# Kernel optimization log

Hardware: AMD Instinct MI355X
Metric: run time of the kernel (lower is better)

The kernel has to match this reference:

```python
import jax, jax.numpy as jnp
import numpy as np

B, L, N, H, HU = 512, 16, 10000, 128, 128

def _rn(k, shape, s=0.05):
    return jax.random.normal(k, shape, jnp.float32) * s

def setup_inputs():
    ks = jax.random.split(jax.random.key(0), 26)
    return dict(
        x=jax.random.normal(ks[0], (B, 2), jnp.float32),
        t0_res=jax.random.normal(ks[1], (B, 1), jnp.float32),
        node_inputs=jax.random.normal(ks[2], (B, 2 * L, N), jnp.float32),
        tau_inputs=jax.random.normal(ks[3], (B, L, 1), jnp.float32),
        end=jax.random.normal(ks[4], (B, 2), jnp.float32),
        coords=jax.random.normal(ks[5], (B, 2 * L, 2), jnp.float32),
        Wx1=_rn(ks[6], (1, 2)), Wx2=_rn(ks[7], (H, 1)), bx2=_rn(ks[8], (H,)),
        Wres=_rn(ks[9], (H, 1)), bres=_rn(ks[10], (H,)),
        Wnode=_rn(ks[11], (H, N)),
        Wtau=_rn(ks[12], (H, 1)), btau=_rn(ks[13], (H,)),
        Wend1=_rn(ks[14], (1, 2)), Wend2=_rn(ks[15], (H, 1)), bend2=_rn(ks[16], (H,)),
        Wcoord=_rn(ks[17], (H, 2)),
        lstm_Wih=_rn(ks[18], (7, 4 * H, H)), lstm_Whh=_rn(ks[19], (7, 4 * H, H)),
        lstm_bih=_rn(ks[20], (7, 4 * H)), lstm_bhh=_rn(ks[21], (7, 4 * H)),
        head_W1=_rn(ks[22], (7, HU, H)), head_b1=_rn(ks[23], (7, HU)),
        head_W2=_rn(ks[24], (7, 1, HU)), head_b2=_rn(ks[25], (7, 1)),
    )

def _lstm_last(s, Wih, Whh, bih, bhh):
    # s: [T, B, H] (time-first, like torch LSTM default). PyTorch gate order: i, f, g, o.
    h0 = jnp.zeros((s.shape[1], Whh.shape[1]), s.dtype)
    def step(carry, xt):
        h, c = carry
        g = xt @ Wih.T + h @ Whh.T + (bih + bhh)
        i, f, gg, o = jnp.split(g, 4, axis=-1)
        c = jax.nn.sigmoid(f) * c + jax.nn.sigmoid(i) * jnp.tanh(gg)
        h = jax.nn.sigmoid(o) * jnp.tanh(c)
        return (h, c), None
    (h, _), _ = jax.lax.scan(step, (h0, h0), s)
    return h  # last output == last hidden state

def _forward(x, t0_res, node_inputs, tau_inputs, end, coords,
             Wx1, Wx2, bx2, Wres, bres, Wnode, Wtau, btau,
             Wend1, Wend2, bend2, Wcoord,
             lstm_Wih, lstm_Whh, lstm_bih, lstm_bhh,
             head_W1, head_b1, head_W2, head_b2):
    xh = jnp.tanh((x @ Wx1.T) @ Wx2.T + bx2)        # [B,H]
    t0h = jnp.tanh(t0_res @ Wres.T + bres)          # [B,H]
    nodeh = node_inputs @ Wnode.T                   # [B,2L,H] (dominant memory-bound GEMM)
    tauh = jnp.tanh(tau_inputs @ Wtau.T + btau)     # [B,L,H]
    endh = (end @ Wend1.T) @ Wend2.T + bend2        # [B,H]
    coordh = coords @ Wcoord.T                      # [B,2L,H]
    ne, no = nodeh[:, 0::2], nodeh[:, 1::2]         # even/odd walk nodes [B,L,H]
    ce, co = coordh[:, 0::2], coordh[:, 1::2]
    def interleave(parts):  # k x [B,L,H] -> time-first [k*L, B, H], per-step order preserved
        s = jnp.stack(parts, axis=2)
        return jnp.swapaxes(s.reshape(s.shape[0], -1, s.shape[-1]), 0, 1)
    pre = jnp.stack([xh, t0h], axis=0)  # [2,B,H]
    suf = endh[None]                    # [1,B,H]
    seqs = [
        jnp.concatenate([pre, interleave([tauh, ne, ce, no, co]), suf], 0),  # all        T=5L+3
        jnp.concatenate([pre, interleave([tauh]), suf], 0),                  # time       T=L+3
        jnp.swapaxes(nodeh, 0, 1),                                           # node       T=2L
        jnp.swapaxes(coordh, 0, 1),                                          # coord      T=2L
        jnp.concatenate([pre, interleave([tauh, ne, no]), suf], 0),          # node_time  T=3L+3
        interleave([ne, ce, no, co]),                                        # node_coord T=4L
        jnp.concatenate([pre, interleave([tauh, ce, co]), suf], 0),          # time_coord T=3L+3
    ]
    outs = []
    for k, s in enumerate(seqs):
        h = _lstm_last(s, lstm_Wih[k], lstm_Whh[k], lstm_bih[k], lstm_bhh[k])
        outs.append(jnp.tanh(h @ head_W1[k].T + head_b1[k]) @ head_W2[k].T + head_b2[k])
    return tuple(outs)  # matches torch return order: all, time, node, coord, node_time, node_coord, time_coord

def reference(x, t0_res, node_inputs, tau_inputs, end, coords,
              Wx1, Wx2, bx2, Wres, bres, Wnode, Wtau, btau,
              Wend1, Wend2, bend2, Wcoord,
              lstm_Wih, lstm_Whh, lstm_bih, lstm_bhh,
              head_W1, head_b1, head_W2, head_b2):
    return _forward(x, t0_res, node_inputs, tau_inputs, end, coords,
                    Wx1, Wx2, bx2, Wres, bres, Wnode, Wtau, btau,
                    Wend1, Wend2, bend2, Wcoord,
                    lstm_Wih, lstm_Whh, lstm_bih, lstm_bhh,
                    head_W1, head_b1, head_W2, head_b2)
```

## Files before the change

kernel.cpp:

```cpp
#include <hip/hip_runtime.h>
#include <hip/hip_fp16.h>

typedef _Float16 f16;
typedef _Float16 f16x8 __attribute__((ext_vector_type(8)));
typedef float f32x4 __attribute__((ext_vector_type(4)));

#define NB 512
#define NL 16
#define NK 10000
#define NH 128
#define NSF 316
#define NT128 79

__device__ __forceinline__ float fast_exp2(float x) {
#if __has_builtin(__builtin_amdgcn_exp2f)
  return __builtin_amdgcn_exp2f(x);
#else
  return exp2f(x);
#endif
}
__device__ __forceinline__ float fast_rcp(float x) {
#if __has_builtin(__builtin_amdgcn_rcpf)
  return __builtin_amdgcn_rcpf(x);
#else
  return 1.f / x;
#endif
}
__device__ __forceinline__ float sigf(float x) {
  return fast_rcp(1.f + fast_exp2(-1.44269504f * x));
}
__device__ __forceinline__ float tanh_fast(float x) {
  return 2.f * fast_rcp(1.f + fast_exp2(-2.88539008f * x)) - 1.f;
}

__device__ __forceinline__ void gload16(const void* g, void* l) {
  __builtin_amdgcn_global_load_lds(
      (const __attribute__((address_space(1))) unsigned int*)g,
      (__attribute__((address_space(3))) unsigned int*)l, 16, 0, 0);
}

__global__ void prep_kernel(
    const float* __restrict__ x, const float* __restrict__ t0,
    const float* __restrict__ tau, const float* __restrict__ endi,
    const float* __restrict__ coords,
    const float* __restrict__ Wx1, const float* __restrict__ Wx2,
    const float* __restrict__ bx2, const float* __restrict__ Wres,
    const float* __restrict__ bres, const float* __restrict__ Wnode,
    const float* __restrict__ Wtau, const float* __restrict__ btau,
    const float* __restrict__ Wend1, const float* __restrict__ Wend2,
    const float* __restrict__ bend2, const float* __restrict__ Wcoord,
    const float* __restrict__ Wih, const float* __restrict__ Whh,
    const float* __restrict__ bih, const float* __restrict__ bhh,
    f16* __restrict__ xh, f16* __restrict__ t0h, f16* __restrict__ endh,
    f16* __restrict__ tauh, f16* __restrict__ coordh, f16* __restrict__ Wf,
    f16* __restrict__ Wih16, f16* __restrict__ Whh16, float* __restrict__ bsum) {
  const int tid0 = blockIdx.x * blockDim.x + threadIdx.x;
  const int stride = gridDim.x * blockDim.x;

  const int nWf = NSF * 4096;
  const int nW = 7 * 512 * NH;
  const int nb = 7 * 512;
  const int nxh = NB * NH;
  const int ntau = NB * NL * NH;
  const int nco = NB * 2 * NL * NH;

  for (int i = tid0; i < nWf; i += stride) {
    const int s = i >> 12, r = i & 4095;
    const int nt = r >> 9, l2 = r & 511;
    const int lane = l2 >> 3, e = l2 & 7;
    const int kg = lane >> 4, lr = lane & 15;
    const int col = nt * 16 + lr;
    const int k = s * 32 + kg * 8 + e;
    Wf[i] = (k < NK) ? (f16)Wnode[(size_t)col * NK + k] : (f16)0.f;
  }
  for (int i = tid0; i < nW; i += stride) {
    Wih16[i] = (f16)Wih[i];
    Whh16[i] = (f16)Whh[i];
  }
  for (int i = tid0; i < nb; i += stride) bsum[i] = bih[i] + bhh[i];
  for (int i = tid0; i < nxh; i += stride) {
    const int b = i >> 7, h = i & 127;
    const float s = x[2 * b] * Wx1[0] + x[2 * b + 1] * Wx1[1];
    xh[i] = (f16)tanhf(s * Wx2[h] + bx2[h]);
    t0h[i] = (f16)tanhf(t0[b] * Wres[h] + bres[h]);
    const float e = endi[2 * b] * Wend1[0] + endi[2 * b + 1] * Wend1[1];
    endh[i] = (f16)(e * Wend2[h] + bend2[h]);
  }
  for (int i = tid0; i < ntau; i += stride) {
    const int h = i & 127, bl = i >> 7;
    tauh[i] = (f16)tanhf(tau[bl] * Wtau[h] + btau[h]);
  }
  for (int i = tid0; i < nco; i += stride) {
    const int h = i & 127, br = i >> 7;
    coordh[i] = (f16)(coords[2 * br] * Wcoord[2 * h] +
                      coords[2 * br + 1] * Wcoord[2 * h + 1]);
  }
}

__global__ __launch_bounds__(512, 2) void node_gemm(const float* __restrict__ A,
                                                    const f16* __restrict__ Wf,
                                                    f16* __restrict__ Cn) {
  __shared__ char lds[4][32768];
  const int tid = threadIdx.x;
  const int w = tid >> 6, l = tid & 63;
  const int lr = l & 15, kg = l >> 4;
  const int r0 = blockIdx.x * 64;
  char* lds0 = &lds[0][0];

  const char* ap[4];
  int bnd[4];
#pragma unroll
  for (int i = 0; i < 4; i++) {
    const int row = w * 8 + i * 2 + (l >> 5);
    const int bswz = ((l & 31) * 16) ^ ((row & 7) << 4);
    ap[i] = (const char*)A + (size_t)(r0 + row) * 40000 + bswz;
    bnd[i] = 39984 - bswz;
  }

  const int cp = w >> 1;
  const int kw = w & 1;
  int rdoA[4][2][2];
#pragma unroll
  for (int rg = 0; rg < 4; rg++) {
    const int row = rg * 16 + lr;
    const int s = (row & 7) << 4;
#pragma unroll
    for (int ks = 0; ks < 2; ks++)
#pragma unroll
      for (int h = 0; h < 2; h++)
        rdoA[rg][ks][h] =
            row * 512 + ((kw * 256 + ks * 128 + kg * 32 + h * 16) ^ s);
  }

  f32x4 acc[4][2];
#pragma unroll
  for (int rg = 0; rg < 4; rg++)
#pragma unroll
    for (int j = 0; j < 2; j++) {
      f32x4 z = {0.f, 0.f, 0.f, 0.f};
      acc[rg][j] = z;
    }

  auto burst = [&](int ta) {
    const int tb0 = ta * 512, tb1 = tb0 + 512;
    char* d0 = lds0 + (ta & 3) * 32768 + w * 4096;
    char* d1 = lds0 + ((ta + 1) & 3) * 32768 + w * 4096;
    const bool two = (ta + 1 < NT128);
#pragma unroll
    for (int i = 0; i < 4; i++) {
      gload16(ap[i] + (tb0 < bnd[i] ? tb0 : bnd[i]), d0 + i * 1024);
      if (two) gload16(ap[i] + (tb1 < bnd[i] ? tb1 : bnd[i]), d1 + i * 1024);
    }
  };

  auto loadB = [&](int t, f16x8 (&B)[2][2]) {
    const f16* bp = Wf + (size_t)(4 * t + 2 * kw) * 4096 + cp * 1024 + l * 8;
#pragma unroll
    for (int j = 0; j < 2; j++)
#pragma unroll
      for (int ks = 0; ks < 2; ks++)
        B[j][ks] = *(const f16x8*)(bp + (size_t)ks * 4096 + j * 512);
  };

  auto compute = [&](int t, const f16x8 (&B)[2][2]) {
    const char* cb = lds0 + (t & 3) * 32768;
#pragma unroll
    for (int ks = 0; ks < 2; ks++)
#pragma unroll
      for (int rg = 0; rg < 4; rg++) {
        const f32x4 a0 = *(const f32x4*)(cb + rdoA[rg][ks][0]);
        const f32x4 a1 = *(const f32x4*)(cb + rdoA[rg][ks][1]);
        f16x8 af;
        af[0] = (f16)a0[0]; af[1] = (f16)a0[1];
        af[2] = (f16)a0[2]; af[3] = (f16)a0[3];
        af[4] = (f16)a1[0]; af[5] = (f16)a1[1];
        af[6] = (f16)a1[2]; af[7] = (f16)a1[3];
#pragma unroll
        for (int j = 0; j < 2; j++)
          acc[rg][j] =
              __builtin_amdgcn_mfma_f32_16x16x32_f16(af, B[j][ks], acc[rg][j], 0, 0, 0);
      }
  };

  f16x8 BA[2][2], BB[2][2];

  burst(0);
  loadB(0, BA);

  for (int e = 0; e < NT128 - 1; e += 2) {
    asm volatile("s_waitcnt vmcnt(4)" ::: "memory");
    __builtin_amdgcn_s_barrier();
    loadB(e + 1, BB);
    burst(e + 2);
    compute(e, BA);
    loadB(e + 2, BA);
    compute(e + 1, BB);
  }
  asm volatile("s_waitcnt vmcnt(0)" ::: "memory");
  __builtin_amdgcn_s_barrier();
  compute(78, BA);

  if (kw == 1) {
#pragma unroll
    for (int rg = 0; rg < 4; rg++)
#pragma unroll
      for (int j = 0; j < 2; j++) {
        const int tl = (cp * 4 + rg) * 2 + j;
        *(f32x4*)(lds0 + tl * 1024 + l * 16) = acc[rg][j];
      }
  }
  __syncthreads();
  if (kw == 0) {
#pragma unroll
    for (int rg = 0; rg < 4; rg++)
#pragma unroll
      for (int j = 0; j < 2; j++) {
        const int tl = (cp * 4 + rg) * 2 + j;
        const f32x4 p = *(const f32x4*)(lds0 + tl * 1024 + l * 16);
        const f32x4 s = acc[rg][j] + p;
        f16* crow =
            Cn + (size_t)(r0 + rg * 16 + kg * 4) * NH + cp * 32 + j * 16 + lr;
#pragma unroll
        for (int jr = 0; jr < 4; jr++) crow[(size_t)jr * NH] = (f16)s[jr];
      }
  }
}

__global__ __launch_bounds__(512, 2) void lstm_run(
    const f16* __restrict__ xh, const f16* __restrict__ t0h,
    const f16* __restrict__ endh, const f16* __restrict__ tauh,
    const f16* __restrict__ nodeh, const f16* __restrict__ coordh,
    const f16* __restrict__ Wih16, const f16* __restrict__ Whh16,
    const float* __restrict__ bsum, const float* __restrict__ hW1,
    const float* __restrict__ hb1, const float* __restrict__ hW2,
    const float* __restrict__ hb2, float* __restrict__ out) {
  __shared__ f16 hbuf[2][16 * NH];
  __shared__ float hu[16 * NH];

  const int k = blockIdx.x >> 5;
  const int b0 = (blockIdx.x & 31) << 4;
  const int w = threadIdx.x >> 6;
  const int l = threadIdx.x & 63;
  const int lr = l & 15, kg = l >> 4;

  int len;
  switch (k) {
    case 0: len = 83; break;
    case 1: len = 19; break;
    case 2: len = 32; break;
    case 3: len = 32; break;
    case 4: len = 51; break;
    case 5: len = 64; break;
    default: len = 51; break;
  }

  auto xptr = [&](int t) -> const f16* {
    const f16* cb; int bstr, idx;
    if (k == 2) { cb = nodeh; bstr = 32 * NH; idx = t; }
    else if (k == 3) { cb = coordh; bstr = 32 * NH; idx = t; }
    else if (k == 5) {
      const int q = t >> 2, r = t & 3;
      cb = (r == 0 || r == 2) ? nodeh : coordh;
      bstr = 32 * NH;
      idx = 2 * q + ((r >= 2) ? 1 : 0);
    } else {
      if (t == 0) { cb = xh; bstr = NH; idx = 0; }
      else if (t == 1) { cb = t0h; bstr = NH; idx = 0; }
      else if (t == len - 1) { cb = endh; bstr = NH; idx = 0; }
      else {
        const int u = t - 2;
        if (k == 0) {
          const int q = u / 5, r = u - 5 * q;
          if (r == 0) { cb = tauh; bstr = 16 * NH; idx = q; }
          else if (r == 1) { cb = nodeh; bstr = 32 * NH; idx = 2 * q; }
          else if (r == 2) { cb = coordh; bstr = 32 * NH; idx = 2 * q; }
          else if (r == 3) { cb = nodeh; bstr = 32 * NH; idx = 2 * q + 1; }
          else { cb = coordh; bstr = 32 * NH; idx = 2 * q + 1; }
        } else if (k == 1) { cb = tauh; bstr = 16 * NH; idx = u; }
        else if (k == 4) {
          const int q = u / 3, r = u - 3 * q;
          if (r == 0) { cb = tauh; bstr = 16 * NH; idx = q; }
          else { cb = nodeh; bstr = 32 * NH; idx = 2 * q + (r - 1); }
        } else {
          const int q = u / 3, r = u - 3 * q;
          if (r == 0) { cb = tauh; bstr = 16 * NH; idx = q; }
          else { cb = coordh; bstr = 32 * NH; idx = 2 * q + (r - 1); }
        }
      }
    }
    return cb + (size_t)(b0 + lr) * bstr + idx * NH + kg * 8;
  };

  f16x8 Wh[4][4], Wi[4][4];
  float bias[4];
  {
    const f16* whb = Whh16 + (size_t)k * 512 * NH;
    const f16* wib = Wih16 + (size_t)k * 512 * NH;
#pragma unroll
    for (int g = 0; g < 4; g++) {
      const int col = g * 128 + w * 16 + lr;
      bias[g] = bsum[k * 512 + col];
#pragma unroll
      for (int kc = 0; kc < 4; kc++) {
        Wh[kc][g] = *(const f16x8*)(whb + (size_t)col * NH + kc * 32 + kg * 8);
        Wi[kc][g] = *(const f16x8*)(wib + (size_t)col * NH + kc * 32 + kg * 8);
      }
    }
  }

  char* lds0 = (char*)&hbuf[0][0];
  *(unsigned long long*)(lds0 + threadIdx.x * 8) = 0ull;
  __syncthreads();

  float c[4] = {0, 0, 0, 0};

  int rdo[4];
#pragma unroll
  for (int kc = 0; kc < 4; kc++) {
    const int colb = (kc * 32 + kg * 8) * 2;
    rdo[kc] = lr * 256 + (colb ^ ((lr & 7) << 4));
  }
  int wro[4];
#pragma unroll
  for (int jr = 0; jr < 4; jr++) {
    const int hrow = kg * 4 + jr;
    const int hcol = w * 16 + lr;
    wro[jr] = hrow * 256 + ((hcol * 2) ^ ((hrow & 7) << 4));
  }

  f16x8 axc[4];
  {
    const f16* xp = xptr(0);
#pragma unroll
    for (int kc = 0; kc < 4; kc++) axc[kc] = *(const f16x8*)(xp + kc * 32);
  }

  int cur = 0;
  for (int t = 0; t < len; t++) {
    char* rb = lds0 + cur * 4096;
    f16x8 ah[4];
#pragma unroll
    for (int kc = 0; kc < 4; kc++) ah[kc] = *(const f16x8*)(rb + rdo[kc]);

    f16x8 axn[4];
    if (t + 1 < len) {
      const f16* xp = xptr(t + 1);
#pragma unroll
      for (int kc = 0; kc < 4; kc++) axn[kc] = *(const f16x8*)(xp + kc * 32);
    }

    f32x4 acc[4];
#pragma unroll
    for (int g = 0; g < 4; g++) {
      f32x4 binit = {bias[g], bias[g], bias[g], bias[g]};
      acc[g] = binit;
    }
#pragma unroll
    for (int kc = 0; kc < 4; kc++)
#pragma unroll
      for (int g = 0; g < 4; g++)
        acc[g] = __builtin_amdgcn_mfma_f32_16x16x32_f16(axc[kc], Wi[kc][g], acc[g], 0, 0, 0);
#pragma unroll
    for (int kc = 0; kc < 4; kc++)
#pragma unroll
      for (int g = 0; g < 4; g++)
        acc[g] = __builtin_amdgcn_mfma_f32_16x16x32_f16(ah[kc], Wh[kc][g], acc[g], 0, 0, 0);

    char* wb = lds0 + (cur ^ 1) * 4096;
#pragma unroll
    for (int jr = 0; jr < 4; jr++) {
      const float iv = acc[0][jr];
      const float fv = acc[1][jr];
      const float gv = acc[2][jr];
      const float ov = acc[3][jr];
      const float cn = sigf(fv) * c[jr] + sigf(iv) * tanh_fast(gv);
      c[jr] = cn;
      const float hn = sigf(ov) * tanh_fast(cn);
      *(f16*)(wb + wro[jr]) = (f16)hn;
    }
    __syncthreads();
#pragma unroll
    for (int kc = 0; kc < 4; kc++) axc[kc] = axn[kc];
    cur ^= 1;
  }

  {
    char* rb = lds0 + cur * 4096;
    f16x8 ah[4];
#pragma unroll
    for (int kc = 0; kc < 4; kc++) ah[kc] = *(const f16x8*)(rb + rdo[kc]);
    const float* W1 = hW1 + (size_t)k * NH * NH;
    const int col = w * 16 + lr;
    f32x4 hacc;
    {
      const float b1 = hb1[k * NH + col];
      f32x4 binit = {b1, b1, b1, b1};
      hacc = binit;
    }
#pragma unroll
    for (int kc = 0; kc < 4; kc++) {
      const float* wrow = W1 + (size_t)col * NH + kc * 32 + kg * 8;
      const f32x4 w0 = *(const f32x4*)(wrow);
      const f32x4 w1 = *(const f32x4*)(wrow + 4);
      f16x8 wv;
      wv[0] = (f16)w0[0]; wv[1] = (f16)w0[1]; wv[2] = (f16)w0[2]; wv[3] = (f16)w0[3];
      wv[4] = (f16)w1[0]; wv[5] = (f16)w1[1]; wv[6] = (f16)w1[2]; wv[7] = (f16)w1[3];
      hacc = __builtin_amdgcn_mfma_f32_16x16x32_f16(ah[kc], wv, hacc, 0, 0, 0);
    }
#pragma unroll
    for (int jr = 0; jr < 4; jr++)
      hu[(kg * 4 + jr) * NH + col] = tanh_fast(hacc[jr]);
  }
  __syncthreads();
  if (w == 0) {
    const int b = l >> 2, part = l & 3;
    const float* W2 = hW2 + (size_t)k * NH;
    float s = 0.f;
#pragma unroll
    for (int j = 0; j < 32; j++)
      s += hu[b * NH + part * 32 + j] * W2[part * 32 + j];
    s += __shfl_xor(s, 1);
    s += __shfl_xor(s, 2);
    if (part == 0) out[k * NB + b0 + b] = s + hb2[k];
  }
}

extern "C" void kernel_launch(void* const* d_in, const int* in_sizes, int n_in,
                              void* d_out, int out_size, void* d_ws, size_t ws_size,
                              hipStream_t stream) {
  (void)in_sizes; (void)n_in; (void)out_size; (void)ws_size;
  const float* x = (const float*)d_in[0];
  const float* t0 = (const float*)d_in[1];
  const float* node = (const float*)d_in[2];
  const float* tau = (const float*)d_in[3];
  const float* endi = (const float*)d_in[4];
  const float* coords = (const float*)d_in[5];
  const float* Wx1 = (const float*)d_in[6];
  const float* Wx2 = (const float*)d_in[7];
  const float* bx2 = (const float*)d_in[8];
  const float* Wres = (const float*)d_in[9];
  const float* bres = (const float*)d_in[10];
  const float* Wnode = (const float*)d_in[11];
  const float* Wtau = (const float*)d_in[12];
  const float* btau = (const float*)d_in[13];
  const float* Wend1 = (const float*)d_in[14];
  const float* Wend2 = (const float*)d_in[15];
  const float* bend2 = (const float*)d_in[16];
  const float* Wcoord = (const float*)d_in[17];
  const float* Wih = (const float*)d_in[18];
  const float* Whh = (const float*)d_in[19];
  const float* bih = (const float*)d_in[20];
  const float* bhh = (const float*)d_in[21];
  const float* hW1 = (const float*)d_in[22];
  const float* hb1 = (const float*)d_in[23];
  const float* hW2 = (const float*)d_in[24];
  const float* hb2 = (const float*)d_in[25];

  char* ws = (char*)d_ws;
  f16* xh = (f16*)ws;      ws += (size_t)NB * NH * 2;
  f16* t0h = (f16*)ws;     ws += (size_t)NB * NH * 2;
  f16* endh = (f16*)ws;    ws += (size_t)NB * NH * 2;
  f16* tauh = (f16*)ws;    ws += (size_t)NB * NL * NH * 2;
  f16* nodeh = (f16*)ws;   ws += (size_t)NB * 2 * NL * NH * 2;
  f16* coordh = (f16*)ws;  ws += (size_t)NB * 2 * NL * NH * 2;
  f16* Wf = (f16*)ws;      ws += (size_t)NSF * 4096 * 2;
  f16* Wih16 = (f16*)ws;   ws += (size_t)7 * 512 * NH * 2;
  f16* Whh16 = (f16*)ws;   ws += (size_t)7 * 512 * NH * 2;
  float* bsum = (float*)ws;

  prep_kernel<<<1024, 256, 0, stream>>>(
      x, t0, tau, endi, coords, Wx1, Wx2, bx2, Wres, bres, Wnode, Wtau, btau,
      Wend1, Wend2, bend2, Wcoord, Wih, Whh, bih, bhh,
      xh, t0h, endh, tauh, coordh, Wf, Wih16, Whh16, bsum);
  node_gemm<<<256, 512, 0, stream>>>(node, Wf, nodeh);
  lstm_run<<<224, 512, 0, stream>>>(xh, t0h, endh, tauh, nodeh, coordh,
                                    Wih16, Whh16, bsum, hW1, hb1, hW2, hb2,
                                    (float*)d_out);
}
```

Measured before the change: 266.9 us.

## Split node GEMM along K across two blocks with fp32 partials and reduce kernel

The node projection GEMM now splits the K dimension in half, launching twice as many blocks (512 instead of 256). Each block processes half the k-tiles with smaller 64-wide LDS stages and a higher occupancy launch bound, then writes fp32 partial sums to a workspace. A new reduce kernel adds the two partials and converts the result to fp16. This is meant to fill more CUs and raise occupancy on this memory-bound GEMM, at the cost of an extra launch and extra fp32 partial-sum traffic.

```diff
diff --git a/kernel.cpp b/kernel.cpp
--- a/kernel.cpp
+++ b/kernel.cpp
@@ -3,6 +3,7 @@
 
 typedef _Float16 f16;
 typedef _Float16 f16x8 __attribute__((ext_vector_type(8)));
+typedef _Float16 f16x4 __attribute__((ext_vector_type(4)));
 typedef float f32x4 __attribute__((ext_vector_type(4)));
 
 #define NB 512
@@ -10,7 +11,6 @@
 #define NK 10000
 #define NH 128
 #define NSF 316
-#define NT128 79
 
 __device__ __forceinline__ float fast_exp2(float x) {
 #if __has_builtin(__builtin_amdgcn_exp2f)
@@ -97,39 +97,40 @@
   }
 }
 
-__global__ __launch_bounds__(512, 2) void node_gemm(const float* __restrict__ A,
+__global__ __launch_bounds__(512, 4) void node_gemm(const float* __restrict__ A,
                                                     const f16* __restrict__ Wf,
-                                                    f16* __restrict__ Cn) {
-  __shared__ char lds[4][32768];
+                                                    float* __restrict__ P) {
+  __shared__ char lds[4][16384];
   const int tid = threadIdx.x;
   const int w = tid >> 6, l = tid & 63;
   const int lr = l & 15, kg = l >> 4;
-  const int r0 = blockIdx.x * 64;
+  const int h = blockIdx.x & 1;
+  const int m = blockIdx.x >> 1;
+  const int r0 = m * 64;
+  const int ts = h ? 78 : 0;
+  const int end = h ? 157 : 78;
   char* lds0 = &lds[0][0];
 
-  const char* ap[4];
-  int bnd[4];
-#pragma unroll
-  for (int i = 0; i < 4; i++) {
-    const int row = w * 8 + i * 2 + (l >> 5);
-    const int bswz = ((l & 31) * 16) ^ ((row & 7) << 4);
-    ap[i] = (const char*)A + (size_t)(r0 + row) * 40000 + bswz;
-    bnd[i] = 39984 - bswz;
-  }
-
-  const int cp = w >> 1;
-  const int kw = w & 1;
-  int rdoA[4][2][2];
+  const char* ap[2];
+  int bnd[2];
+#pragma unroll
+  for (int s = 0; s < 2; s++) {
+    const int chunk = s * 512 + w * 64 + l;
+    const int row = chunk >> 4, c = chunk & 15;
+    const int col = (c * 16) ^ ((row & 7) << 4);
+    ap[s] = (const char*)A + (size_t)(r0 + row) * 40000 + col;
+    bnd[s] = 39984 - col;
+  }
+
+  const int kw = w & 1, cp = w >> 1;
+  int rdoA[4][2];
 #pragma unroll
   for (int rg = 0; rg < 4; rg++) {
     const int row = rg * 16 + lr;
-    const int s = (row & 7) << 4;
-#pragma unroll
-    for (int ks = 0; ks < 2; ks++)
-#pragma unroll
-      for (int h = 0; h < 2; h++)
-        rdoA[rg][ks][h] =
-            row * 512 + ((kw * 256 + ks * 128 + kg * 32 + h * 16) ^ s);
+    const int sw = (row & 7) << 4;
+#pragma unroll
+    for (int hh = 0; hh < 2; hh++)
+      rdoA[rg][hh] = row * 256 + ((kw * 128 + kg * 32 + hh * 16) ^ sw);
   }
 
   f32x4 acc[4][2];
@@ -141,89 +142,107 @@
       acc[rg][j] = z;
     }
 
-  auto burst = [&](int ta) {
-    const int tb0 = ta * 512, tb1 = tb0 + 512;
-    char* d0 = lds0 + (ta & 3) * 32768 + w * 4096;
-    char* d1 = lds0 + ((ta + 1) & 3) * 32768 + w * 4096;
-    const bool two = (ta + 1 < NT128);
-#pragma unroll
-    for (int i = 0; i < 4; i++) {
-      gload16(ap[i] + (tb0 < bnd[i] ? tb0 : bnd[i]), d0 + i * 1024);
-      if (two) gload16(ap[i] + (tb1 < bnd[i] ? tb1 : bnd[i]), d1 + i * 1024);
-    }
+  auto burst1 = [&](int t) {
+    char* db = lds0 + (t & 3) * 16384 + w * 1024;
+    const int tb = t * 256;
+#pragma unroll
+    for (int s = 0; s < 2; s++)
+      gload16(ap[s] + (tb < bnd[s] ? tb : bnd[s]), db + s * 8192);
   };
-
-  auto loadB = [&](int t, f16x8 (&B)[2][2]) {
-    const f16* bp = Wf + (size_t)(4 * t + 2 * kw) * 4096 + cp * 1024 + l * 8;
-#pragma unroll
-    for (int j = 0; j < 2; j++)
-#pragma unroll
-      for (int ks = 0; ks < 2; ks++)
-        B[j][ks] = *(const f16x8*)(bp + (size_t)ks * 4096 + j * 512);
+  auto burst2 = [&](int t) {
+    const int tb0 = t * 256, tb1 = tb0 + 256;
+    char* d0 = lds0 + (t & 3) * 16384 + w * 1024;
+    char* d1 = lds0 + ((t + 1) & 3) * 16384 + w * 1024;
+#pragma unroll
+    for (int s = 0; s < 2; s++) {
+      gload16(ap[s] + (tb0 < bnd[s] ? tb0 : bnd[s]), d0 + s * 8192);
+      gload16(ap[s] + (tb1 < bnd[s] ? tb1 : bnd[s]), d1 + s * 8192);
+    }
   };
 
-  auto compute = [&](int t, const f16x8 (&B)[2][2]) {
-    const char* cb = lds0 + (t & 3) * 32768;
-#pragma unroll
-    for (int ks = 0; ks < 2; ks++)
-#pragma unroll
-      for (int rg = 0; rg < 4; rg++) {
-        const f32x4 a0 = *(const f32x4*)(cb + rdoA[rg][ks][0]);
-        const f32x4 a1 = *(const f32x4*)(cb + rdoA[rg][ks][1]);
-        f16x8 af;
-        af[0] = (f16)a0[0]; af[1] = (f16)a0[1];
-        af[2] = (f16)a0[2]; af[3] = (f16)a0[3];
-        af[4] = (f16)a1[0]; af[5] = (f16)a1[1];
-        af[6] = (f16)a1[2]; af[7] = (f16)a1[3];
-#pragma unroll
-        for (int j = 0; j < 2; j++)
-          acc[rg][j] =
-              __builtin_amdgcn_mfma_f32_16x16x32_f16(af, B[j][ks], acc[rg][j], 0, 0, 0);
-      }
+  auto loadB = [&](int t, f16x8 (&B)[2]) {
+    const f16* bp = Wf + (size_t)(2 * t + kw) * 4096 + cp * 1024 + l * 8;
+#pragma unroll
+    for (int j = 0; j < 2; j++) B[j] = *(const f16x8*)(bp + j * 512);
   };
 
-  f16x8 BA[2][2], BB[2][2];
-
-  burst(0);
-  loadB(0, BA);
-
-  for (int e = 0; e < NT128 - 1; e += 2) {
-    asm volatile("s_waitcnt vmcnt(4)" ::: "memory");
+  auto compute = [&](int t, const f16x8 (&B)[2]) {
+    const char* cb = lds0 + (t & 3) * 16384;
+#pragma unroll
+    for (int rg = 0; rg < 4; rg++) {
+      const f32x4 a0 = *(const f32x4*)(cb + rdoA[rg][0]);
+      const f32x4 a1 = *(const f32x4*)(cb + rdoA[rg][1]);
+      f16x8 af;
+      af[0] = (f16)a0[0]; af[1] = (f16)a0[1];
+      af[2] = (f16)a0[2]; af[3] = (f16)a0[3];
+      af[4] = (f16)a1[0]; af[5] = (f16)a1[1];
+      af[6] = (f16)a1[2]; af[7] = (f16)a1[3];
+#pragma unroll
+      for (int j = 0; j < 2; j++)
+        acc[rg][j] =
+            __builtin_amdgcn_mfma_f32_16x16x32_f16(af, B[j], acc[rg][j], 0, 0, 0);
+    }
+  };
+
+  f16x8 BA[2], BB[2];
+
+  burst2(ts);
+  loadB(ts, BA);
+
+  int e = ts;
+  for (; e + 1 < end; e += 2) {
+    asm volatile("s_waitcnt vmcnt(2)" ::: "memory");
     __builtin_amdgcn_s_barrier();
     loadB(e + 1, BB);
-    burst(e + 2);
+    if (e + 3 < end) burst2(e + 2);
+    else if (e + 2 < end) burst1(e + 2);
     compute(e, BA);
-    loadB(e + 2, BA);
+    if (e + 2 < end) loadB(e + 2, BA);
     compute(e + 1, BB);
   }
-  asm volatile("s_waitcnt vmcnt(0)" ::: "memory");
-  __builtin_amdgcn_s_barrier();
-  compute(78, BA);
-
+  if (e < end) {
+    asm volatile("s_waitcnt vmcnt(0)" ::: "memory");
+    __builtin_amdgcn_s_barrier();
+    compute(e, BA);
+  }
+
+  __syncthreads();
   if (kw == 1) {
 #pragma unroll
     for (int rg = 0; rg < 4; rg++)
 #pragma unroll
       for (int j = 0; j < 2; j++) {
-        const int tl = (cp * 4 + rg) * 2 + j;
+        const int tl = cp * 8 + rg * 2 + j;
         *(f32x4*)(lds0 + tl * 1024 + l * 16) = acc[rg][j];
       }
   }
   __syncthreads();
   if (kw == 0) {
+    float* Ph = P + ((size_t)h << 21);
 #pragma unroll
     for (int rg = 0; rg < 4; rg++)
 #pragma unroll
       for (int j = 0; j < 2; j++) {
-        const int tl = (cp * 4 + rg) * 2 + j;
+        const int tl = cp * 8 + rg * 2 + j;
         const f32x4 p = *(const f32x4*)(lds0 + tl * 1024 + l * 16);
         const f32x4 s = acc[rg][j] + p;
-        f16* crow =
-            Cn + (size_t)(r0 + rg * 16 + kg * 4) * NH + cp * 32 + j * 16 + lr;
-#pragma unroll
-        for (int jr = 0; jr < 4; jr++) crow[(size_t)jr * NH] = (f16)s[jr];
+        float* prow =
+            Ph + (size_t)(r0 + rg * 16 + kg * 4) * NH + cp * 32 + j * 16 + lr;
+#pragma unroll
+        for (int jr = 0; jr < 4; jr++) prow[(size_t)jr * NH] = s[jr];
       }
   }
+}
+
+__global__ __launch_bounds__(256) void reduce2(const float* __restrict__ P,
+                                               f16* __restrict__ Cn) {
+  const int i = blockIdx.x * 256 + threadIdx.x;
+  const size_t o = (size_t)i * 4;
+  f32x4 s = *(const f32x4*)(P + o);
+  s += *(const f32x4*)(P + (1u << 21) + o);
+  f16x4 hv;
+  hv[0] = (f16)s[0]; hv[1] = (f16)s[1]; hv[2] = (f16)s[2]; hv[3] = (f16)s[3];
+  *(f16x4*)(Cn + o) = hv;
 }
 
 __global__ __launch_bounds__(512, 2) void lstm_run(
@@ -466,13 +485,15 @@
   f16* Wf = (f16*)ws;      ws += (size_t)NSF * 4096 * 2;
   f16* Wih16 = (f16*)ws;   ws += (size_t)7 * 512 * NH * 2;
   f16* Whh16 = (f16*)ws;   ws += (size_t)7 * 512 * NH * 2;
-  float* bsum = (float*)ws;
+  float* bsum = (float*)ws; ws += (size_t)7 * 512 * 4;
+  float* Pp = (float*)ws;
 
   prep_kernel<<<1024, 256, 0, stream>>>(
       x, t0, tau, endi, coords, Wx1, Wx2, bx2, Wres, bres, Wnode, Wtau, btau,
       Wend1, Wend2, bend2, Wcoord, Wih, Whh, bih, bhh,
       xh, t0h, endh, tauh, coordh, Wf, Wih16, Whh16, bsum);
-  node_gemm<<<256, 512, 0, stream>>>(node, Wf, nodeh);
+  node_gemm<<<512, 512, 0, stream>>>(node, Wf, Pp);
+  reduce2<<<2048, 256, 0, stream>>>(Pp, nodeh);
   lstm_run<<<224, 512, 0, stream>>>(xh, t0h, endh, tauh, nodeh, coordh,
                                     Wih16, Whh16, bsum, hW1, hb1, hW2, hb2,
                                     (float*)d_out);
```

After: 269.7 us. About the same (+1.1%).

## Retile node GEMM to 32-row blocks with 256-wide K stages, doubling grid

Applied to the files above, without the earlier changes.

The node GEMM block tile shrinks from 64 to 32 rows and each pipeline stage now covers 256 K elements instead of 128, so the grid grows from 256 to 512 blocks and there are 40 stages instead of 79. The padded weight layout grows from 316 to 320 slabs to fit. The goal is more blocks in flight to saturate memory bandwidth on the 164 MB fp32 activation stream and fewer barriers per K. The cost is that weight B-fragments are reloaded from global/L2 twice as often per row, and each thread holds more B registers.

```diff
diff --git a/kernel.cpp b/kernel.cpp
--- a/kernel.cpp
+++ b/kernel.cpp
@@ -9,8 +9,8 @@
 #define NL 16
 #define NK 10000
 #define NH 128
-#define NSF 316
-#define NT128 79
+#define NSF 320
+#define NT 40
 
 __device__ __forceinline__ float fast_exp2(float x) {
 #if __has_builtin(__builtin_amdgcn_exp2f)
@@ -104,70 +104,68 @@
   const int tid = threadIdx.x;
   const int w = tid >> 6, l = tid & 63;
   const int lr = l & 15, kg = l >> 4;
-  const int r0 = blockIdx.x * 64;
+  const int r0 = blockIdx.x * 32;
   char* lds0 = &lds[0][0];
 
   const char* ap[4];
   int bnd[4];
 #pragma unroll
   for (int i = 0; i < 4; i++) {
-    const int row = w * 8 + i * 2 + (l >> 5);
-    const int bswz = ((l & 31) * 16) ^ ((row & 7) << 4);
-    ap[i] = (const char*)A + (size_t)(r0 + row) * 40000 + bswz;
-    bnd[i] = 39984 - bswz;
-  }
-
-  const int cp = w >> 1;
-  const int kw = w & 1;
-  int rdoA[4][2][2];
-#pragma unroll
-  for (int rg = 0; rg < 4; rg++) {
+    const int row = w * 4 + i;
+    const int x0 = (l * 16) ^ ((row & 7) << 4);
+    ap[i] = (const char*)A + (size_t)(r0 + row) * 40000 + x0;
+    bnd[i] = 39984 - x0;
+  }
+
+  const int kw = w & 1, cp = w >> 1;
+  int rdoA[2][4][2];
+#pragma unroll
+  for (int rg = 0; rg < 2; rg++) {
     const int row = rg * 16 + lr;
-    const int s = (row & 7) << 4;
-#pragma unroll
-    for (int ks = 0; ks < 2; ks++)
+    const int sw = (row & 7) << 4;
+#pragma unroll
+    for (int ks = 0; ks < 4; ks++)
 #pragma unroll
       for (int h = 0; h < 2; h++)
         rdoA[rg][ks][h] =
-            row * 512 + ((kw * 256 + ks * 128 + kg * 32 + h * 16) ^ s);
-  }
-
-  f32x4 acc[4][2];
-#pragma unroll
-  for (int rg = 0; rg < 4; rg++)
+            row * 1024 + ((kw * 512 + ks * 128 + kg * 32 + h * 16) ^ sw);
+  }
+
+  f32x4 acc[2][2];
+#pragma unroll
+  for (int rg = 0; rg < 2; rg++)
 #pragma unroll
     for (int j = 0; j < 2; j++) {
       f32x4 z = {0.f, 0.f, 0.f, 0.f};
       acc[rg][j] = z;
     }
 
-  auto burst = [&](int ta) {
-    const int tb0 = ta * 512, tb1 = tb0 + 512;
-    char* d0 = lds0 + (ta & 3) * 32768 + w * 4096;
-    char* d1 = lds0 + ((ta + 1) & 3) * 32768 + w * 4096;
-    const bool two = (ta + 1 < NT128);
+  auto burst = [&](int t) {
+    const int tb0 = t * 1024, tb1 = tb0 + 1024;
+    char* d0 = lds0 + (t & 3) * 32768 + (w * 4) * 1024;
+    char* d1 = lds0 + ((t + 1) & 3) * 32768 + (w * 4) * 1024;
 #pragma unroll
     for (int i = 0; i < 4; i++) {
       gload16(ap[i] + (tb0 < bnd[i] ? tb0 : bnd[i]), d0 + i * 1024);
-      if (two) gload16(ap[i] + (tb1 < bnd[i] ? tb1 : bnd[i]), d1 + i * 1024);
+      gload16(ap[i] + (tb1 < bnd[i] ? tb1 : bnd[i]), d1 + i * 1024);
     }
   };
 
-  auto loadB = [&](int t, f16x8 (&B)[2][2]) {
-    const f16* bp = Wf + (size_t)(4 * t + 2 * kw) * 4096 + cp * 1024 + l * 8;
+  auto loadB = [&](int t, f16x8 (&B)[2][4]) {
+    const f16* bp = Wf + (size_t)(8 * t + 4 * kw) * 4096 + cp * 1024 + l * 8;
 #pragma unroll
     for (int j = 0; j < 2; j++)
 #pragma unroll
-      for (int ks = 0; ks < 2; ks++)
+      for (int ks = 0; ks < 4; ks++)
         B[j][ks] = *(const f16x8*)(bp + (size_t)ks * 4096 + j * 512);
   };
 
-  auto compute = [&](int t, const f16x8 (&B)[2][2]) {
+  auto compute = [&](int t, const f16x8 (&B)[2][4]) {
     const char* cb = lds0 + (t & 3) * 32768;
 #pragma unroll
-    for (int ks = 0; ks < 2; ks++)
-#pragma unroll
-      for (int rg = 0; rg < 4; rg++) {
+    for (int ks = 0; ks < 4; ks++)
+#pragma unroll
+      for (int rg = 0; rg < 2; rg++) {
         const f32x4 a0 = *(const f32x4*)(cb + rdoA[rg][ks][0]);
         const f32x4 a1 = *(const f32x4*)(cb + rdoA[rg][ks][1]);
         f16x8 af;
@@ -177,45 +175,43 @@
         af[6] = (f16)a1[2]; af[7] = (f16)a1[3];
 #pragma unroll
         for (int j = 0; j < 2; j++)
-          acc[rg][j] =
-              __builtin_amdgcn_mfma_f32_16x16x32_f16(af, B[j][ks], acc[rg][j], 0, 0, 0);
+          acc[rg][j] = __builtin_amdgcn_mfma_f32_16x16x32_f16(
+              af, B[j][ks], acc[rg][j], 0, 0, 0);
       }
   };
 
-  f16x8 BA[2][2], BB[2][2];
+  f16x8 BA[2][4], BB[2][4];
 
   burst(0);
   loadB(0, BA);
 
-  for (int e = 0; e < NT128 - 1; e += 2) {
-    asm volatile("s_waitcnt vmcnt(4)" ::: "memory");
+  for (int e = 0; e < NT; e += 2) {
+    asm volatile("s_waitcnt vmcnt(8)" ::: "memory");
     __builtin_amdgcn_s_barrier();
     loadB(e + 1, BB);
-    burst(e + 2);
+    if (e + 2 < NT) burst(e + 2);
     compute(e, BA);
-    loadB(e + 2, BA);
+    if (e + 2 < NT) loadB(e + 2, BA);
     compute(e + 1, BB);
   }
-  asm volatile("s_waitcnt vmcnt(0)" ::: "memory");
-  __builtin_amdgcn_s_barrier();
-  compute(78, BA);
-
+
+  __syncthreads();
   if (kw == 1) {
 #pragma unroll
-    for (int rg = 0; rg < 4; rg++)
+    for (int rg = 0; rg < 2; rg++)
 #pragma unroll
       for (int j = 0; j < 2; j++) {
-        const int tl = (cp * 4 + rg) * 2 + j;
+        const int tl = cp * 4 + rg * 2 + j;
         *(f32x4*)(lds0 + tl * 1024 + l * 16) = acc[rg][j];
       }
   }
   __syncthreads();
   if (kw == 0) {
 #pragma unroll
-    for (int rg = 0; rg < 4; rg++)
+    for (int rg = 0; rg < 2; rg++)
 #pragma unroll
       for (int j = 0; j < 2; j++) {
-        const int tl = (cp * 4 + rg) * 2 + j;
+        const int tl = cp * 4 + rg * 2 + j;
         const f32x4 p = *(const f32x4*)(lds0 + tl * 1024 + l * 16);
         const f32x4 s = acc[rg][j] + p;
         f16* crow =
@@ -472,7 +468,7 @@
       x, t0, tau, endi, coords, Wx1, Wx2, bx2, Wres, bres, Wnode, Wtau, btau,
       Wend1, Wend2, bend2, Wcoord, Wih, Whh, bih, bhh,
       xh, t0h, endh, tauh, coordh, Wf, Wih16, Whh16, bsum);
-  node_gemm<<<256, 512, 0, stream>>>(node, Wf, nodeh);
+  node_gemm<<<512, 512, 0, stream>>>(node, Wf, nodeh);
   lstm_run<<<224, 512, 0, stream>>>(xh, t0h, endh, tauh, nodeh, coordh,
                                     Wih16, Whh16, bsum, hW1, hb1, hW2, hb2,
                                     (float*)d_out);
```

Result: slower. 281.8 us (+5.6%).

## Stage node_gemm A tiles through registers instead of direct global-to-LDS loads

Applied to the files above, without the earlier changes.

Replaces the global_load_lds async copy of A tiles with nontemporal register loads followed by swizzled ds_writes, reworking the software pipeline so one tile is kept in flight in registers. The XOR swizzle is now applied on the LDS write side instead of the global address, which gives contiguous global reads. This adds two barriers per tile and a full vmcnt(0) wait in each half-step, so overlap depth is lower than the previous two-tile bursts. It also uses extra VGPRs for the staging registers.

```diff
diff --git a/kernel.cpp b/kernel.cpp
--- a/kernel.cpp
+++ b/kernel.cpp
@@ -10,7 +10,7 @@
 #define NK 10000
 #define NH 128
 #define NSF 316
-#define NT128 79
+#define NT 79
 
 __device__ __forceinline__ float fast_exp2(float x) {
 #if __has_builtin(__builtin_amdgcn_exp2f)
@@ -31,12 +31,6 @@
 }
 __device__ __forceinline__ float tanh_fast(float x) {
   return 2.f * fast_rcp(1.f + fast_exp2(-2.88539008f * x)) - 1.f;
-}
-
-__device__ __forceinline__ void gload16(const void* g, void* l) {
-  __builtin_amdgcn_global_load_lds(
-      (const __attribute__((address_space(1))) unsigned int*)g,
-      (__attribute__((address_space(3))) unsigned int*)l, 16, 0, 0);
 }
 
 __global__ void prep_kernel(
@@ -108,28 +102,28 @@
   char* lds0 = &lds[0][0];
 
   const char* ap[4];
-  int bnd[4];
+  int bnd[4], wdo[4];
 #pragma unroll
   for (int i = 0; i < 4; i++) {
     const int row = w * 8 + i * 2 + (l >> 5);
-    const int bswz = ((l & 31) * 16) ^ ((row & 7) << 4);
-    ap[i] = (const char*)A + (size_t)(r0 + row) * 40000 + bswz;
-    bnd[i] = 39984 - bswz;
-  }
-
-  const int cp = w >> 1;
-  const int kw = w & 1;
+    const int off = (l & 31) * 16;
+    ap[i] = (const char*)A + (size_t)(r0 + row) * 40000 + off;
+    bnd[i] = 39984 - off;
+    wdo[i] = row * 512 + (off ^ ((row & 7) << 4));
+  }
+
+  const int kw = w & 1, cp = w >> 1;
   int rdoA[4][2][2];
 #pragma unroll
   for (int rg = 0; rg < 4; rg++) {
     const int row = rg * 16 + lr;
-    const int s = (row & 7) << 4;
+    const int sw = (row & 7) << 4;
 #pragma unroll
     for (int ks = 0; ks < 2; ks++)
 #pragma unroll
       for (int h = 0; h < 2; h++)
         rdoA[rg][ks][h] =
-            row * 512 + ((kw * 256 + ks * 128 + kg * 32 + h * 16) ^ s);
+            row * 512 + ((kw * 256 + ks * 128 + kg * 32 + h * 16) ^ sw);
   }
 
   f32x4 acc[4][2];
@@ -141,16 +135,19 @@
       acc[rg][j] = z;
     }
 
-  auto burst = [&](int ta) {
-    const int tb0 = ta * 512, tb1 = tb0 + 512;
-    char* d0 = lds0 + (ta & 3) * 32768 + w * 4096;
-    char* d1 = lds0 + ((ta + 1) & 3) * 32768 + w * 4096;
-    const bool two = (ta + 1 < NT128);
+  auto loadA = [&](int t, f32x4 (&r)[4]) {
+    const int tb = t * 512;
 #pragma unroll
     for (int i = 0; i < 4; i++) {
-      gload16(ap[i] + (tb0 < bnd[i] ? tb0 : bnd[i]), d0 + i * 1024);
-      if (two) gload16(ap[i] + (tb1 < bnd[i] ? tb1 : bnd[i]), d1 + i * 1024);
-    }
+      const int off = tb < bnd[i] ? tb : bnd[i];
+      r[i] = __builtin_nontemporal_load((const f32x4*)(ap[i] + off));
+    }
+  };
+
+  auto dswrite = [&](int t, const f32x4 (&r)[4]) {
+    char* db = lds0 + (t & 3) * 32768;
+#pragma unroll
+    for (int i = 0; i < 4; i++) *(f32x4*)(db + wdo[i]) = r[i];
   };
 
   auto loadB = [&](int t, f16x8 (&B)[2][2]) {
@@ -177,35 +174,47 @@
         af[6] = (f16)a1[2]; af[7] = (f16)a1[3];
 #pragma unroll
         for (int j = 0; j < 2; j++)
-          acc[rg][j] =
-              __builtin_amdgcn_mfma_f32_16x16x32_f16(af, B[j][ks], acc[rg][j], 0, 0, 0);
+          acc[rg][j] = __builtin_amdgcn_mfma_f32_16x16x32_f16(
+              af, B[j][ks], acc[rg][j], 0, 0, 0);
       }
   };
 
+  f32x4 RA[4], RB[4];
   f16x8 BA[2][2], BB[2][2];
 
-  burst(0);
+  loadA(0, RA);
+  asm volatile("s_waitcnt vmcnt(0)" ::: "memory");
+  dswrite(0, RA);
+  loadA(1, RB);
   loadB(0, BA);
-
-  for (int e = 0; e < NT128 - 1; e += 2) {
-    asm volatile("s_waitcnt vmcnt(4)" ::: "memory");
+  asm volatile("s_waitcnt lgkmcnt(0)" ::: "memory");
+  __builtin_amdgcn_s_barrier();
+
+  for (int e = 0; e + 1 < NT; e += 2) {
+    asm volatile("s_waitcnt vmcnt(0)" ::: "memory");
+    dswrite(e + 1, RB);
+    loadA(e + 2, RA);
+    loadB(e + 1, BB);
+    asm volatile("s_waitcnt lgkmcnt(0)" ::: "memory");
     __builtin_amdgcn_s_barrier();
-    loadB(e + 1, BB);
-    burst(e + 2);
     compute(e, BA);
+    asm volatile("s_waitcnt vmcnt(0)" ::: "memory");
+    dswrite(e + 2, RA);
+    if (e + 3 < NT) loadA(e + 3, RB);
     loadB(e + 2, BA);
+    asm volatile("s_waitcnt lgkmcnt(0)" ::: "memory");
+    __builtin_amdgcn_s_barrier();
     compute(e + 1, BB);
   }
-  asm volatile("s_waitcnt vmcnt(0)" ::: "memory");
-  __builtin_amdgcn_s_barrier();
-  compute(78, BA);
-
+  compute(NT - 1, BA);
+
+  __syncthreads();
   if (kw == 1) {
 #pragma unroll
     for (int rg = 0; rg < 4; rg++)
 #pragma unroll
       for (int j = 0; j < 2; j++) {
-        const int tl = (cp * 4 + rg) * 2 + j;
+        const int tl = cp * 8 + rg * 2 + j;
         *(f32x4*)(lds0 + tl * 1024 + l * 16) = acc[rg][j];
       }
   }
@@ -215,7 +224,7 @@
     for (int rg = 0; rg < 4; rg++)
 #pragma unroll
       for (int j = 0; j < 2; j++) {
-        const int tl = (cp * 4 + rg) * 2 + j;
+        const int tl = cp * 8 + rg * 2 + j;
         const f32x4 p = *(const f32x4*)(lds0 + tl * 1024 + l * 16);
         const f32x4 s = acc[rg][j] + p;
         f16* crow =
```

Measured after the change: 250.1 us. 1.07x faster.
